# Kernel tuning notes

Measured on AMD Instinct MI355X. Metric: run time of the kernel, lower is better.

Reference implementation:

```python
import jax, jax.numpy as jnp
import numpy as np
from jax import lax

K = 3        # kernel_size
PAD = 1      # padding
STRIDE = 1   # stride


def conv2d(x, w, stride, pad):
    return lax.conv_general_dilated(
        x, w, (stride, stride), [(pad, pad), (pad, pad)],
        dimension_numbers=('NCHW', 'OIHW', 'NCHW'))


def setup_inputs() -> dict:
    key = jax.random.key(0)
    ks = jax.random.split(key, 8)
    B, Ci, Cc, H, W = 8, 64, 64, 128, 128
    K2 = K * K
    return {
        'x_img': jax.random.normal(ks[0], (B, Ci, H, W), jnp.float32),
        'x_cont': jax.random.normal(ks[1], (B, Cc, H, W), jnp.float32),
        'w_fuse': jax.random.normal(ks[2], (Ci, Ci + Cc, 1, 1), jnp.float32) * 0.05,
        'w_off': jax.random.normal(ks[3], (2 * K2, Ci, K, K), jnp.float32) * 0.01,
        'b_off': jax.random.normal(ks[4], (2 * K2,), jnp.float32) * 0.1,
        'w_mod': jax.random.normal(ks[5], (K2, Ci, K, K), jnp.float32) * 0.01,
        'b_mod': jax.random.normal(ks[6], (K2,), jnp.float32) * 0.1,
        'w_reg': jax.random.normal(ks[7], (Ci, Ci, K, K), jnp.float32) * 0.05,
    }


def _bilinear_sample(img, py, px):
    # Zero padding outside the image (per-corner validity, matches torchvision).
    C, Hin, Win = img.shape
    flat = img.reshape(C, -1)
    y0 = jnp.floor(py)
    x0 = jnp.floor(px)

    def gather(yy, xx):
        valid = (yy >= 0) & (yy <= Hin - 1) & (xx >= 0) & (xx <= Win - 1)
        yc = jnp.clip(yy, 0, Hin - 1).astype(jnp.int32)
        xc = jnp.clip(xx, 0, Win - 1).astype(jnp.int32)
        return flat[:, yc * Win + xc] * valid[None].astype(img.dtype)

    wy1 = py - y0; wy0 = 1.0 - wy1
    wx1 = px - x0; wx0 = 1.0 - wx1
    return (gather(y0, x0) * (wy0 * wx0)[None]
            + gather(y0, x0 + 1.0) * (wy0 * wx1)[None]
            + gather(y0 + 1.0, x0) * (wy1 * wx0)[None]
            + gather(y0 + 1.0, x0 + 1.0) * (wy1 * wx1)[None])


def reference(x_img, x_cont, w_fuse, w_off, b_off, w_mod, b_mod, w_reg):
    # 1x1 fuse of image features with control factor
    x = conv2d(jnp.concatenate([x_img, x_cont], axis=1), w_fuse, 1, 0)
    # offset / modulator branches
    off = conv2d(x, w_off, STRIDE, PAD) + b_off[None, :, None, None]
    mod = 2.0 * jax.nn.sigmoid(conv2d(x, w_mod, STRIDE, PAD) + b_mod[None, :, None, None])
    B, C, Hin, Win = x.shape
    K2 = K * K
    Hout, Wout = off.shape[2], off.shape[3]
    # torchvision layout: channel 2k = dy, 2k+1 = dx for kernel pos k = i*K + j
    off = off.reshape(B, K2, 2, Hout, Wout)
    dy, dx = off[:, :, 0], off[:, :, 1]
    ky = (jnp.arange(K2) // K).astype(x.dtype)
    kx = (jnp.arange(K2) % K).astype(x.dtype)
    base_y = (jnp.arange(Hout) * STRIDE - PAD).astype(x.dtype)
    base_x = (jnp.arange(Wout) * STRIDE - PAD).astype(x.dtype)
    py = dy + base_y[None, None, :, None] + ky[None, :, None, None]  # [B,K2,H,W]
    px = dx + base_x[None, None, None, :] + kx[None, :, None, None]
    sampled = jax.vmap(_bilinear_sample)(x, py, px)          # [B,C,K2,H,W]
    sampled = sampled * mod[:, None]                          # modulation
    out = jnp.einsum('oik,bikhw->bohw', w_reg.reshape(C, C, K2), sampled)
    return out
```

## Files before the change

### kernel.cpp

```cpp
#include <hip/hip_runtime.h>
#include <math.h>

#define B_   8
#define C_   64
#define H_   128
#define W_   128
#define HW_  16384
#define K2_  9

typedef float f32x4 __attribute__((ext_vector_type(4)));
typedef short bf16x8 __attribute__((ext_vector_type(8)));
typedef unsigned short u16x4 __attribute__((ext_vector_type(4)));

#define WS_WRP  8192
#define WS_WRP2 26624
#define WS_XT   45056
#define WS_OM   8433664

static __device__ __forceinline__ unsigned short f2bf(float x) {
    unsigned int u = __float_as_uint(x);
    unsigned int r = (u + 0x7fffu + ((u >> 16) & 1u)) >> 16;
    return (unsigned short)r;
}
static __device__ __forceinline__ float bf2f(unsigned short u) {
    return __uint_as_float(((unsigned int)u) << 16);
}

__global__ __launch_bounds__(256) void k_fuse(const float* __restrict__ xi,
                                              const float* __restrict__ xc,
                                              const float* __restrict__ wf,
                                              const float* __restrict__ wreg,
                                              const float* __restrict__ wOff,
                                              const float* __restrict__ wMod,
                                              unsigned short* __restrict__ xtb,
                                              unsigned short* __restrict__ wrP,
                                              unsigned short* __restrict__ wrP2) {
    __shared__ unsigned short sA[1024 * 8];
    const int t = threadIdx.x;
    const int lane = t & 63;
    const int wv = t >> 6;
    const int b = blockIdx.x & 7;
    const int yh = blockIdx.x >> 3;
    const int y = yh >> 1;
    const int h = yh & 1;

    if (blockIdx.x < 18) {
        const int idx = blockIdx.x * 256 + t;
        if (idx < 4608) {
            int ln = idx & 63, mt = (idx >> 6) & 3, kc = (idx >> 8) & 1, tap = idx >> 9;
            int o = mt * 16 + (ln & 15);
            int ibase = kc * 32 + (ln >> 4) * 8;
#pragma unroll
            for (int j = 0; j < 8; ++j)
                wrP[idx * 8 + j] = f2bf(wreg[(o * 64 + ibase + j) * 9 + tap]);
        }
        if (idx < 2304) {
            int ln = idx & 63, mt = (idx >> 6) & 1, kc = idx >> 7;
            int m = mt * 16 + (ln & 15);
            int gkb = kc * 32 + (ln >> 4) * 8;
#pragma unroll
            for (int j = 0; j < 8; ++j) {
                int gk = gkb + j, tap = gk >> 6, ci = gk & 63;
                float v = 0.f;
                if (m < 18)      v = wOff[(m * 64 + ci) * 9 + tap];
                else if (m < 27) v = wMod[((m - 18) * 64 + ci) * 9 + tap];
                wrP2[idx * 8 + j] = f2bf(v);
            }
        }
    }

#pragma unroll
    for (int r = 0; r < 4; ++r) {
        const int c = t + 256 * r;
        const int f = c >> 6;
        const int ln = c & 63;
        const int mt = f & 3, kc = f >> 2;
        const int m = mt * 16 + (ln & 15);
        const int kb = kc * 32 + (ln >> 4) * 8;
        const float* s = wf + m * 128 + kb;
        unsigned short us[8];
#pragma unroll
        for (int j = 0; j < 8; ++j) us[j] = f2bf(s[j]);
        *(bf16x8*)&sA[c * 8] = *(const bf16x8*)us;
    }
    __syncthreads();

    const int n15 = lane & 15;
    const int q4 = lane >> 4;
    const int px = h * 64 + wv * 16 + n15;
    const size_t poff = (size_t)y * W_ + px;

    f32x4 acc[4];
#pragma unroll
    for (int mt = 0; mt < 4; ++mt) acc[mt] = (f32x4){0.f, 0.f, 0.f, 0.f};

#pragma unroll
    for (int kc = 0; kc < 4; ++kc) {
        const float* src = (kc < 2)
            ? (xi + ((size_t)(b * 64 + kc * 32 + q4 * 8)) * HW_ + poff)
            : (xc + ((size_t)(b * 64 + (kc - 2) * 32 + q4 * 8)) * HW_ + poff);
        unsigned short us[8];
#pragma unroll
        for (int j = 0; j < 8; ++j) us[j] = f2bf(src[(size_t)j * HW_]);
        const bf16x8 bf = *(const bf16x8*)us;
#pragma unroll
        for (int mt = 0; mt < 4; ++mt) {
            const bf16x8 a = *(const bf16x8*)&sA[((kc * 4 + mt) * 64 + lane) * 8];
            acc[mt] = __builtin_amdgcn_mfma_f32_16x16x32_bf16(a, bf, acc[mt], 0, 0, 0);
        }
    }

#pragma unroll
    for (int mt = 0; mt < 4; ++mt) {
        u16x4 o4;
        o4.x = f2bf(acc[mt][0]); o4.y = f2bf(acc[mt][1]);
        o4.z = f2bf(acc[mt][2]); o4.w = f2bf(acc[mt][3]);
        *(u16x4*)&xtb[((size_t)b * HW_ + poff) * 64 + mt * 16 + q4 * 4] = o4;
    }
}

__global__ __launch_bounds__(256) void k_offmod(const unsigned short* __restrict__ xtb,
                                                const unsigned short* __restrict__ wrP2,
                                                const float* __restrict__ bOff,
                                                const float* __restrict__ bMod,
                                                float* __restrict__ om) {
    __shared__ unsigned short sB[3 * 66 * 72];
    const int t = threadIdx.x;
    const int lane = t & 63;
    const int wv = t >> 6;
    const int b = blockIdx.x & 7;
    const int yh = blockIdx.x >> 3;
    const int y = yh >> 1;
    const int h = yh & 1;

    for (int idx = t; idx < 3 * 66 * 8; idx += 256) {
        const int c8 = idx & 7;
        const int pp = (idx >> 3) % 66;
        const int row = (idx >> 3) / 66;
        const int gx = h * 64 + pp - 1;
        const int gy = y + row - 1;
        bf16x8 v = {0, 0, 0, 0, 0, 0, 0, 0};
        if (gx >= 0 && gx < W_ && gy >= 0 && gy < H_)
            v = *(const bf16x8*)&xtb[(((size_t)(b * H_ + gy)) * W_ + gx) * 64 + c8 * 8];
        *(bf16x8*)&sB[(row * 66 + pp) * 72 + c8 * 8] = v;
    }
    __syncthreads();

    const int n15 = lane & 15;
    const int q4 = lane >> 4;

    f32x4 acc[2];
    acc[0] = (f32x4){0.f, 0.f, 0.f, 0.f};
    acc[1] = (f32x4){0.f, 0.f, 0.f, 0.f};

#pragma unroll
    for (int kc = 0; kc < 18; ++kc) {
        const int gkb = kc * 32 + q4 * 8;
        const int tap = gkb >> 6;
        const int ci = gkb & 63;
        const int row = tap / 3, kx = tap % 3;
        const bf16x8 bf = *(const bf16x8*)&sB[(row * 66 + (wv * 16 + n15 + kx)) * 72 + ci];
        const bf16x8 a0 = *(const bf16x8*)(wrP2 + (((size_t)(kc * 2 + 0) * 64 + lane) * 8));
        const bf16x8 a1 = *(const bf16x8*)(wrP2 + (((size_t)(kc * 2 + 1) * 64 + lane) * 8));
        acc[0] = __builtin_amdgcn_mfma_f32_16x16x32_bf16(a0, bf, acc[0], 0, 0, 0);
        acc[1] = __builtin_amdgcn_mfma_f32_16x16x32_bf16(a1, bf, acc[1], 0, 0, 0);
    }

    const int px = h * 64 + wv * 16 + n15;
    const size_t rec = ((size_t)(b * H_ + y)) * 28 * 128;
#pragma unroll
    for (int mt = 0; mt < 2; ++mt)
#pragma unroll
        for (int r = 0; r < 4; ++r) {
            const int o = mt * 16 + q4 * 4 + r;
            if (o < 18) {
                const int c = (o >> 1) + ((o & 1) ? 9 : 0);
                om[rec + c * 128 + px] = acc[mt][r] + bOff[o];
            } else if (o < 27) {
                const float z = acc[mt][r] + bMod[o - 18];
                om[rec + (18 + (o - 18)) * 128 + px] = 2.f / (1.f + __expf(-z));
            }
        }
}

__global__ __launch_bounds__(256) void k_deform(const unsigned short* __restrict__ xtb,
                                                const float* __restrict__ om,
                                                const unsigned short* __restrict__ wrP,
                                                float* __restrict__ out) {
    __shared__ unsigned short sS2[8 * 520];
    const int t = threadIdx.x;
    const int lane = t & 63;
    const int wv = t >> 6;
    const int b = blockIdx.x & 7;
    const int yh = blockIdx.x >> 3;
    const int y = yh >> 1;
    const int h = yh & 1;

    const char* xbB = (const char*)(xtb + (size_t)b * HW_ * 64);
    const float* omr = om + ((size_t)(b * H_ + y)) * 28 * 128;

    const int n15 = lane & 15;
    const int q4 = lane >> 4;
    const int pA = lane >> 2;
    const int corner = lane & 3;
    const int cy = corner >> 1, cx = corner & 1;
    const int pxA = h * 64 + wv * 16 + pA;
    const int gwrite = (lane >> 3) * 520 + (lane & 7);

    f32x4 acc[4];
#pragma unroll
    for (int mt = 0; mt < 4; ++mt) acc[mt] = (f32x4){0.f, 0.f, 0.f, 0.f};

    for (int k = 0; k < 9; ++k) {
        const int ky = k / 3 - 1, kx = k % 3 - 1;

        int rOff;
        int rW;
        {
            const float dy = omr[k * 128 + pxA];
            const float dxv = omr[(9 + k) * 128 + pxA];
            const float m = omr[(18 + k) * 128 + pxA];
            const float py  = (float)(y + ky) + dy;
            const float pxe = (float)(pxA + kx) + dxv;
            const float y0f = floorf(py), x0f = floorf(pxe);
            const int y0i = (int)y0f, x0i = (int)x0f;
            const float wy1 = py - y0f, wx1 = pxe - x0f;
            const int yy = y0i + cy;
            const int xx = x0i + cx;
            const bool ok = (yy >= 0) && (yy < H_) && (xx >= 0) && (xx < W_);
            const int yc = min(max(yy, 0), H_ - 1);
            const int xc = min(max(xx, 0), W_ - 1);
            const float w = (cy ? wy1 : 1.f - wy1) * (cx ? wx1 : 1.f - wx1) * m;
            rOff = (yc * W_ + xc) * 128;
            rW = (int)__float_as_uint(ok ? w : 0.f);
        }

#pragma unroll
        for (int p = 0; p < 16; ++p) {
            const int l0 = p * 4;
            const unsigned o0 = (unsigned)__builtin_amdgcn_readlane(rOff, l0 + 0);
            const unsigned o1 = (unsigned)__builtin_amdgcn_readlane(rOff, l0 + 1);
            const unsigned o2 = (unsigned)__builtin_amdgcn_readlane(rOff, l0 + 2);
            const unsigned o3 = (unsigned)__builtin_amdgcn_readlane(rOff, l0 + 3);
            const float w0 = __uint_as_float((unsigned)__builtin_amdgcn_readlane(rW, l0 + 0));
            const float w1 = __uint_as_float((unsigned)__builtin_amdgcn_readlane(rW, l0 + 1));
            const float w2 = __uint_as_float((unsigned)__builtin_amdgcn_readlane(rW, l0 + 2));
            const float w3 = __uint_as_float((unsigned)__builtin_amdgcn_readlane(rW, l0 + 3));
            const unsigned short* b0 = (const unsigned short*)(xbB + o0);
            const unsigned short* b1 = (const unsigned short*)(xbB + o1);
            const unsigned short* b2 = (const unsigned short*)(xbB + o2);
            const unsigned short* b3 = (const unsigned short*)(xbB + o3);
            const float v = bf2f(b0[lane]) * w0 + bf2f(b1[lane]) * w1
                          + bf2f(b2[lane]) * w2 + bf2f(b3[lane]) * w3;
            sS2[gwrite + (wv * 16 + p) * 8] = f2bf(v);
        }

#pragma unroll
        for (int kc = 0; kc < 2; ++kc) {
            const bf16x8 bf = *(const bf16x8*)&sS2[(kc * 4 + q4) * 520 + (wv * 16 + n15) * 8];
#pragma unroll
            for (int mt = 0; mt < 4; ++mt) {
                const bf16x8 a = *(const bf16x8*)(wrP +
                    ((((size_t)((k * 2 + kc) * 4 + mt)) * 64 + lane) * 8));
                acc[mt] = __builtin_amdgcn_mfma_f32_16x16x32_bf16(a, bf, acc[mt], 0, 0, 0);
            }
        }
    }

    const int px = h * 64 + wv * 16 + n15;
#pragma unroll
    for (int mt = 0; mt < 4; ++mt)
#pragma unroll
        for (int r = 0; r < 4; ++r) {
            const int o = mt * 16 + q4 * 4 + r;
            out[(((size_t)(b * 64 + o)) * H_ + y) * W_ + px] = acc[mt][r];
        }
}

extern "C" void kernel_launch(void* const* d_in, const int* in_sizes, int n_in,
                              void* d_out, int out_size, void* d_ws, size_t ws_size,
                              hipStream_t stream) {
    const float* x_img  = (const float*)d_in[0];
    const float* x_cont = (const float*)d_in[1];
    const float* w_fuse = (const float*)d_in[2];
    const float* w_off  = (const float*)d_in[3];
    const float* b_off  = (const float*)d_in[4];
    const float* w_mod  = (const float*)d_in[5];
    const float* b_mod  = (const float*)d_in[6];
    const float* w_reg  = (const float*)d_in[7];
    float* out = (float*)d_out;

    float* ws  = (float*)d_ws;
    unsigned short* wrP  = (unsigned short*)(ws + WS_WRP);
    unsigned short* wrP2 = (unsigned short*)(ws + WS_WRP2);
    unsigned short* xtb  = (unsigned short*)(ws + WS_XT);
    float* om  = ws + WS_OM;

    k_fuse<<<B_ * H_ * 2, 256, 0, stream>>>(x_img, x_cont, w_fuse, w_reg, w_off,
                                            w_mod, xtb, wrP, wrP2);
    k_offmod<<<B_ * H_ * 2, 256, 0, stream>>>(xtb, wrP2, b_off, b_mod, om);
    k_deform<<<B_ * H_ * 2, 256, 0, stream>>>(xtb, om, wrP, out);
}
```

Baseline: 216.5 us.

## Fuse offset/modulator conv into deformable sampling kernel via shared memory

Merges the offset/modulator convolution kernel and the deformable conv kernel into one, with each block computing its row-half's offsets and modulators into shared memory instead of a global buffer. This removes one kernel launch and the global write/read of the 28-channel om tensor. Shared memory is reused across phases (halo tile, then offsets, then sample staging), which needs an extra barrier. The larger shared footprint of the halo tile may lower occupancy for the sampling phase.

```diff
diff --git a/kernel.cpp b/kernel.cpp
--- a/kernel.cpp
+++ b/kernel.cpp
@@ -15,7 +15,6 @@
 #define WS_WRP  8192
 #define WS_WRP2 26624
 #define WS_XT   45056
-#define WS_OM   8433664
 
 static __device__ __forceinline__ unsigned short f2bf(float x) {
     unsigned int u = __float_as_uint(x);
@@ -119,12 +118,17 @@
     }
 }
 
-__global__ __launch_bounds__(256) void k_offmod(const unsigned short* __restrict__ xtb,
-                                                const unsigned short* __restrict__ wrP2,
-                                                const float* __restrict__ bOff,
-                                                const float* __restrict__ bMod,
-                                                float* __restrict__ om) {
-    __shared__ unsigned short sB[3 * 66 * 72];
+__global__ __launch_bounds__(256) void k_main(const unsigned short* __restrict__ xtb,
+                                              const unsigned short* __restrict__ wrP,
+                                              const unsigned short* __restrict__ wrP2,
+                                              const float* __restrict__ bOff,
+                                              const float* __restrict__ bMod,
+                                              float* __restrict__ out) {
+    __shared__ char smem[3 * 66 * 72 * 2];
+    unsigned short* sB  = (unsigned short*)smem;
+    float*          sOM = (float*)smem;
+    unsigned short* sS2 = (unsigned short*)(smem + 8192);
+
     const int t = threadIdx.x;
     const int lane = t & 63;
     const int wv = t >> 6;
@@ -132,6 +136,9 @@
     const int yh = blockIdx.x >> 3;
     const int y = yh >> 1;
     const int h = yh & 1;
+
+    const int n15 = lane & 15;
+    const int q4 = lane >> 4;
 
     for (int idx = t; idx < 3 * 66 * 8; idx += 256) {
         const int c8 = idx & 7;
@@ -146,13 +153,9 @@
     }
     __syncthreads();
 
-    const int n15 = lane & 15;
-    const int q4 = lane >> 4;
-
-    f32x4 acc[2];
-    acc[0] = (f32x4){0.f, 0.f, 0.f, 0.f};
-    acc[1] = (f32x4){0.f, 0.f, 0.f, 0.f};
-
+    f32x4 oacc[2];
+    oacc[0] = (f32x4){0.f, 0.f, 0.f, 0.f};
+    oacc[1] = (f32x4){0.f, 0.f, 0.f, 0.f};
 #pragma unroll
     for (int kc = 0; kc < 18; ++kc) {
         const int gkb = kc * 32 + q4 * 8;
@@ -162,49 +165,34 @@
         const bf16x8 bf = *(const bf16x8*)&sB[(row * 66 + (wv * 16 + n15 + kx)) * 72 + ci];
         const bf16x8 a0 = *(const bf16x8*)(wrP2 + (((size_t)(kc * 2 + 0) * 64 + lane) * 8));
         const bf16x8 a1 = *(const bf16x8*)(wrP2 + (((size_t)(kc * 2 + 1) * 64 + lane) * 8));
-        acc[0] = __builtin_amdgcn_mfma_f32_16x16x32_bf16(a0, bf, acc[0], 0, 0, 0);
-        acc[1] = __builtin_amdgcn_mfma_f32_16x16x32_bf16(a1, bf, acc[1], 0, 0, 0);
-    }
-
-    const int px = h * 64 + wv * 16 + n15;
-    const size_t rec = ((size_t)(b * H_ + y)) * 28 * 128;
-#pragma unroll
-    for (int mt = 0; mt < 2; ++mt)
-#pragma unroll
-        for (int r = 0; r < 4; ++r) {
-            const int o = mt * 16 + q4 * 4 + r;
-            if (o < 18) {
-                const int c = (o >> 1) + ((o & 1) ? 9 : 0);
-                om[rec + c * 128 + px] = acc[mt][r] + bOff[o];
-            } else if (o < 27) {
-                const float z = acc[mt][r] + bMod[o - 18];
-                om[rec + (18 + (o - 18)) * 128 + px] = 2.f / (1.f + __expf(-z));
+        oacc[0] = __builtin_amdgcn_mfma_f32_16x16x32_bf16(a0, bf, oacc[0], 0, 0, 0);
+        oacc[1] = __builtin_amdgcn_mfma_f32_16x16x32_bf16(a1, bf, oacc[1], 0, 0, 0);
+    }
+    __syncthreads();
+
+    {
+        const int pxl = wv * 16 + n15;
+#pragma unroll
+        for (int mt = 0; mt < 2; ++mt)
+#pragma unroll
+            for (int r = 0; r < 4; ++r) {
+                const int o = mt * 16 + q4 * 4 + r;
+                if (o < 18) {
+                    const int c = (o >> 1) + ((o & 1) ? 9 : 0);
+                    sOM[c * 64 + pxl] = oacc[mt][r] + bOff[o];
+                } else if (o < 27) {
+                    const float z = oacc[mt][r] + bMod[o - 18];
+                    sOM[(18 + (o - 18)) * 64 + pxl] = 2.f / (1.f + __expf(-z));
+                }
             }
-        }
-}
-
-__global__ __launch_bounds__(256) void k_deform(const unsigned short* __restrict__ xtb,
-                                                const float* __restrict__ om,
-                                                const unsigned short* __restrict__ wrP,
-                                                float* __restrict__ out) {
-    __shared__ unsigned short sS2[8 * 520];
-    const int t = threadIdx.x;
-    const int lane = t & 63;
-    const int wv = t >> 6;
-    const int b = blockIdx.x & 7;
-    const int yh = blockIdx.x >> 3;
-    const int y = yh >> 1;
-    const int h = yh & 1;
+    }
 
     const char* xbB = (const char*)(xtb + (size_t)b * HW_ * 64);
-    const float* omr = om + ((size_t)(b * H_ + y)) * 28 * 128;
-
-    const int n15 = lane & 15;
-    const int q4 = lane >> 4;
     const int pA = lane >> 2;
     const int corner = lane & 3;
     const int cy = corner >> 1, cx = corner & 1;
-    const int pxA = h * 64 + wv * 16 + pA;
+    const int pxAl = wv * 16 + pA;
+    const int pxA = h * 64 + pxAl;
     const int gwrite = (lane >> 3) * 520 + (lane & 7);
 
     f32x4 acc[4];
@@ -217,9 +205,9 @@
         int rOff;
         int rW;
         {
-            const float dy = omr[k * 128 + pxA];
-            const float dxv = omr[(9 + k) * 128 + pxA];
-            const float m = omr[(18 + k) * 128 + pxA];
+            const float dy = sOM[k * 64 + pxAl];
+            const float dxv = sOM[(9 + k) * 64 + pxAl];
+            const float m = sOM[(18 + k) * 64 + pxAl];
             const float py  = (float)(y + ky) + dy;
             const float pxe = (float)(pxA + kx) + dxv;
             const float y0f = floorf(py), x0f = floorf(pxe);
@@ -294,10 +282,8 @@
     unsigned short* wrP  = (unsigned short*)(ws + WS_WRP);
     unsigned short* wrP2 = (unsigned short*)(ws + WS_WRP2);
     unsigned short* xtb  = (unsigned short*)(ws + WS_XT);
-    float* om  = ws + WS_OM;
 
     k_fuse<<<B_ * H_ * 2, 256, 0, stream>>>(x_img, x_cont, w_fuse, w_reg, w_off,
                                             w_mod, xtb, wrP, wrP2);
-    k_offmod<<<B_ * H_ * 2, 256, 0, stream>>>(xtb, wrP2, b_off, b_mod, om);
-    k_deform<<<B_ * H_ * 2, 256, 0, stream>>>(xtb, om, wrP, out);
-}
+    k_main<<<B_ * H_ * 2, 256, 0, stream>>>(xtb, wrP, wrP2, b_off, b_mod, out);
+}
```

Measured after the change: 262.2 us. 21.1% more time.
